# Kernel optimization log

Hardware: AMD Instinct MI355X
Metric: run time of the kernel (lower is better)

The kernel has to match this reference:

```python
import jax, jax.numpy as jnp
import numpy as np

DECAY = 0.6
GAIN = 0.4


def _layernorm(x, g, b, eps=1e-5):
    m = x.mean(-1, keepdims=True)
    v = x.var(-1, keepdims=True)
    return (x - m) * jax.lax.rsqrt(v + eps) * g + b


def _ema_scan(x, axis, reverse=False):
    # linear recurrence state = 0.6*state + 0.4*x as an associative scan
    a = jnp.full_like(x, DECAY)
    b = GAIN * x
    def comb(c1, c2):
        a1, b1 = c1
        a2, b2 = c2
        return a1 * a2, a2 * b1 + b2
    _, y = jax.lax.associative_scan(comb, (a, b), axis=axis, reverse=reverse)
    return y


def setup_inputs() -> dict:
    key = jax.random.key(0)
    B, H, W, D = 16, 64, 64, 384
    inner = 2 * D
    hidden = 4 * D
    ks = jax.random.split(key, 12)
    s = 0.02
    return {
        "x": jax.random.normal(ks[0], (B, H, W, D), jnp.float32),
        "n1_g": jnp.ones((D,), jnp.float32),
        "n1_b": jnp.zeros((D,), jnp.float32),
        "w_in": s * jax.random.normal(ks[1], (D, inner), jnp.float32),
        "b_in": jnp.zeros((inner,), jnp.float32),
        "k_conv": s * jax.random.normal(ks[2], (3, 3, 1, inner), jnp.float32),  # depthwise HWIO
        "on_g": jnp.ones((inner,), jnp.float32),
        "on_b": jnp.zeros((inner,), jnp.float32),
        "w_out": s * jax.random.normal(ks[3], (inner, D), jnp.float32),
        "b_out": jnp.zeros((D,), jnp.float32),
        "n2_g": jnp.ones((D,), jnp.float32),
        "n2_b": jnp.zeros((D,), jnp.float32),
        "w1": s * jax.random.normal(ks[4], (D, hidden), jnp.float32),
        "b1": jnp.zeros((hidden,), jnp.float32),
        "w2": s * jax.random.normal(ks[5], (hidden, D), jnp.float32),
        "b2": jnp.zeros((D,), jnp.float32),
    }


def reference(x, n1_g, n1_b, w_in, b_in, k_conv, on_g, on_b, w_out, b_out,
              n2_g, n2_b, w1, b1, w2, b2):
    inner = w_in.shape[1]
    # --- LegacyScan2DOperator branch ---
    h = _layernorm(x, n1_g, n1_b)
    p = h @ w_in + b_in  # [B,H,W,inner]
    local = jax.lax.conv_general_dilated(
        p, k_conv, window_strides=(1, 1), padding="SAME",
        dimension_numbers=("NHWC", "HWIO", "NHWC"),
        feature_group_count=inner)
    lr = _ema_scan(local, axis=2)                 # left->right over W
    rl = _ema_scan(local, axis=2, reverse=True)   # right->left
    tb = _ema_scan(local, axis=1)                 # top->bottom over H
    bt = _ema_scan(local, axis=1, reverse=True)   # bottom->top
    mixed = 0.25 * (lr + rl + tb + bt) + local
    mixed = _layernorm(mixed, on_g, on_b)
    x = x + (mixed @ w_out + b_out)
    # --- MLP branch ---
    h2 = _layernorm(x, n2_g, n2_b)
    m = jax.nn.gelu(h2 @ w1 + b1, approximate=False) @ w2 + b2
    return x + m
```

## Files before the change

kernel.cpp:

```cpp
#include <hip/hip_runtime.h>
#include <math.h>


typedef __attribute__((ext_vector_type(8))) short bf16x8;
typedef __attribute__((ext_vector_type(4))) float f32x4;

#define T_TOKENS 65536
#define DMODEL 384
#define DINNER 768
#define DHIDDEN 1536

__device__ __forceinline__ float bf2f(unsigned short u) {
  unsigned int x = ((unsigned int)u) << 16;
  return __builtin_bit_cast(float, x);
}
__device__ __forceinline__ unsigned short f2bf(float f) {
  unsigned int x = __builtin_bit_cast(unsigned int, f);
  x += 0x7fffu + ((x >> 16) & 1u);
  return (unsigned short)(x >> 16);
}
__device__ __forceinline__ void unpack2(unsigned int u, float& lo, float& hi) {
  lo = __builtin_bit_cast(float, u << 16);
  hi = __builtin_bit_cast(float, u & 0xffff0000u);
}
__device__ __forceinline__ unsigned int pack2(float lo, float hi) {
  return (unsigned int)f2bf(lo) | ((unsigned int)f2bf(hi) << 16);
}

__device__ __forceinline__ void gload16(const void* g, void* l) {
  __builtin_amdgcn_global_load_lds(
      (const __attribute__((address_space(1))) void*)g,
      (__attribute__((address_space(3))) void*)l, 16, 0, 0);
}

__global__ __launch_bounds__(256) void ln_fused_f32_384(
    const float* __restrict__ in, const float* __restrict__ g,
    const float* __restrict__ b, unsigned short* __restrict__ out) {
  const int tok = blockIdx.x * 4 + (threadIdx.x >> 6);
  const int lane = threadIdx.x & 63;
  const float2* row = (const float2*)(in + (size_t)tok * 384);
  float2 v[3];
  float s = 0.f, ss = 0.f;
#pragma unroll
  for (int k = 0; k < 3; k++) {
    v[k] = row[lane + 64 * k];
    s += v[k].x + v[k].y;
    ss += v[k].x * v[k].x + v[k].y * v[k].y;
  }
#pragma unroll
  for (int off = 32; off > 0; off >>= 1) {
    s += __shfl_xor(s, off);
    ss += __shfl_xor(ss, off);
  }
  const float m = s * (1.0f / 384.0f);
  const float r = rsqrtf(ss * (1.0f / 384.0f) - m * m + 1e-5f);
  unsigned int* op = (unsigned int*)(out + (size_t)tok * 384);
#pragma unroll
  for (int k = 0; k < 3; k++) {
    const int c = lane + 64 * k;
    const float2 gg = ((const float2*)g)[c];
    const float2 bb = ((const float2*)b)[c];
    op[c] = pack2((v[k].x - m) * r * gg.x + bb.x, (v[k].y - m) * r * gg.y + bb.y);
  }
}

__global__ __launch_bounds__(256) void ln_bundle_768(
    const uint4* __restrict__ mixed, const float* __restrict__ g,
    const float* __restrict__ b, uint4* __restrict__ out) {
  const int tid = threadIdx.x;
  const int tk = tid >> 2, j = tid & 3;
  const int token = blockIdx.x * 64 + tk;
  const int bb_ = token >> 12, posb = token & 4095;
  const size_t slab = (size_t)bb_ * 4096 + posb;
  float s = 0.f, ss = 0.f;
#pragma unroll 1
  for (int cg = j; cg < 96; cg += 4) {
    const uint4 v = mixed[((size_t)cg * 16) * 4096 + slab];
    float e0, e1, e2, e3, e4, e5, e6, e7;
    unpack2(v.x, e0, e1); unpack2(v.y, e2, e3);
    unpack2(v.z, e4, e5); unpack2(v.w, e6, e7);
    s += (e0 + e1) + (e2 + e3) + (e4 + e5) + (e6 + e7);
    ss += e0 * e0 + e1 * e1 + e2 * e2 + e3 * e3 + e4 * e4 + e5 * e5 +
          e6 * e6 + e7 * e7;
  }
  s += __shfl_xor(s, 1); ss += __shfl_xor(ss, 1);
  s += __shfl_xor(s, 2); ss += __shfl_xor(ss, 2);
  const float m = s * (1.0f / 768.0f);
  const float r = rsqrtf(ss * (1.0f / 768.0f) - m * m + 1e-5f);
  const size_t tokbase = (size_t)token * 96;
#pragma unroll 1
  for (int cg = j; cg < 96; cg += 4) {
    const uint4 v = mixed[((size_t)cg * 16) * 4096 + slab];
    const float4 g0 = *(const float4*)(g + cg * 8);
    const float4 g1 = *(const float4*)(g + cg * 8 + 4);
    const float4 b0 = *(const float4*)(b + cg * 8);
    const float4 b1 = *(const float4*)(b + cg * 8 + 4);
    float e0, e1, e2, e3, e4, e5, e6, e7;
    unpack2(v.x, e0, e1); unpack2(v.y, e2, e3);
    unpack2(v.z, e4, e5); unpack2(v.w, e6, e7);
    uint4 o;
    o.x = pack2((e0 - m) * r * g0.x + b0.x, (e1 - m) * r * g0.y + b0.y);
    o.y = pack2((e2 - m) * r * g0.z + b0.z, (e3 - m) * r * g0.w + b0.w);
    o.z = pack2((e4 - m) * r * g1.x + b1.x, (e5 - m) * r * g1.y + b1.y);
    o.w = pack2((e6 - m) * r * g1.z + b1.z, (e7 - m) * r * g1.w + b1.w);
    out[tokbase + cg] = o;
  }
}

__global__ __launch_bounds__(256) void wprep_kernel(const float* __restrict__ in,
                                                    unsigned short* __restrict__ out,
                                                    int K, int N) {
  __shared__ float t[32][33];
  const int k0 = blockIdx.x * 32, n0 = blockIdx.y * 32;
  const int a = threadIdx.x & 31, b8 = threadIdx.x >> 5;
#pragma unroll
  for (int i = 0; i < 4; i++)
    t[b8 + 8 * i][a] = in[(size_t)(k0 + b8 + 8 * i) * N + n0 + a];
  __syncthreads();
#pragma unroll
  for (int i = 0; i < 4; i++)
    out[(size_t)(n0 + b8 + 8 * i) * K + k0 + a] = f2bf(t[a][b8 + 8 * i]);
}

template <int EPI>
__global__ __launch_bounds__(256) void gemm_bt_kernel(
    const unsigned short* __restrict__ A, int lda,
    const unsigned short* __restrict__ Bt, int ldb, int KT,
    const float* __restrict__ bias, const float* __restrict__ res,
    void* __restrict__ C, int ldc, int nby) {
  __shared__ unsigned short smem[32768];
  char* const smc = (char*)smem;

  const int tid = threadIdx.x;
  const int w = tid >> 6, lane = tid & 63;
  const int cpx = gridDim.x >> 3;
  const int g = blockIdx.x;
  const int sw = (g & 7) * cpx + (g >> 3);
  const int bx = sw / nby, by = sw - bx * nby;
  const int tok0 = bx << 7, n0 = by << 7;

  const int wm = w >> 1, wn = w & 1;
  const int lrow = lane & 15, kgrp = lane >> 4;
  const int cx = lrow & 7;

  const int lr8 = lane >> 3;
  const int kce = ((lane & 7) ^ lr8) << 3;
  const unsigned short* Abase = A + (size_t)(tok0 + w * 32 + lr8) * lda + kce;
  const unsigned short* Bbase = Bt + (size_t)(n0 + w * 32 + lr8) * ldb + kce;

  f32x4 acc[4][4];
#pragma unroll
  for (int i = 0; i < 4; i++)
#pragma unroll
    for (int j = 0; j < 4; j++) {
      f32x4 z = {0.f, 0.f, 0.f, 0.f};
      acc[i][j] = z;
    }

  const int nt = KT >> 6;
#pragma unroll
  for (int i = 0; i < 4; i++) {
    gload16(Abase + (size_t)i * 8 * lda, smc + (w * 4 + i) * 1024);
    gload16(Bbase + (size_t)i * 8 * ldb, smc + 32768 + (w * 4 + i) * 1024);
  }
  __syncthreads();

  int buf = 0;
  for (int t = 0; t < nt; t++) {
    if (t + 1 < nt) {
      const int kt = (t + 1) << 6;
      const int bo = (buf ^ 1) * 16384;
#pragma unroll
      for (int i = 0; i < 4; i++) {
        gload16(Abase + (size_t)i * 8 * lda + kt, smc + bo + (w * 4 + i) * 1024);
        gload16(Bbase + (size_t)i * 8 * ldb + kt,
                smc + 32768 + bo + (w * 4 + i) * 1024);
      }
    }
    bf16x8 af[2][4], bf_[2][4];
    const int bo = buf * 16384;
#pragma unroll
    for (int ks = 0; ks < 2; ks++) {
#pragma unroll
      for (int f = 0; f < 4; f++) {
        const int co = ((ks * 4 + kgrp) ^ cx) << 4;
        af[ks][f] =
            *(const bf16x8*)(smc + bo + (wm * 64 + f * 16 + lrow) * 128 + co);
        bf_[ks][f] = *(const bf16x8*)(smc + 32768 + bo +
                                      (wn * 64 + f * 16 + lrow) * 128 + co);
      }
    }
#pragma unroll
    for (int ks = 0; ks < 2; ks++)
#pragma unroll
      for (int mf = 0; mf < 4; mf++)
#pragma unroll
        for (int nf = 0; nf < 4; nf++)
          acc[mf][nf] = __builtin_amdgcn_mfma_f32_16x16x32_bf16(
              af[ks][mf], bf_[ks][nf], acc[mf][nf], 0, 0, 0);
    __syncthreads();
    buf ^= 1;
  }

  if constexpr (EPI == 3) {
#pragma unroll
    for (int mf = 0; mf < 4; mf++)
#pragma unroll
      for (int nf = 0; nf < 4; nf++) {
        const int cl = wn * 64 + nf * 16 + lrow;
        const float bv = bias[n0 + cl];
#pragma unroll
        for (int r = 0; r < 4; r++) {
          const int tl = wm * 64 + mf * 16 + kgrp * 4 + r;
          smem[(cl >> 3) * 1032 + tl * 8 + (cl & 7)] =
              f2bf(acc[mf][nf][r] + bv);
        }
      }
    __syncthreads();
    const int bb_ = tok0 >> 12, pos0 = tok0 & 4095, cg0 = n0 >> 3;
    uint4* Cb = (uint4*)C;
#pragma unroll
    for (int e = 0; e < 8; e++) {
      const int lin = e * 256 + tid;
      const int cgl = lin >> 7, pp = lin & 127;
      const uint4 v = *(const uint4*)&smem[cgl * 1032 + pp * 8];
      Cb[((size_t)(cg0 + cgl) * 16 + bb_) * 4096 + pos0 + pp] = v;
    }
  } else {
#pragma unroll
    for (int mf = 0; mf < 4; mf++) {
#pragma unroll
      for (int nf = 0; nf < 4; nf++) {
        const int gcol = n0 + wn * 64 + nf * 16 + lrow;
        const float bv = bias ? bias[gcol] : 0.0f;
#pragma unroll
        for (int r = 0; r < 4; r++) {
          const int grow = tok0 + wm * 64 + mf * 16 + kgrp * 4 + r;
          float v = acc[mf][nf][r] + bv;
          const size_t idx = (size_t)grow * ldc + gcol;
          if constexpr (EPI == 1) {
            ((float*)C)[idx] = v + res[idx];
          } else {
            const float z = 1.5957691216057308f * (v + 0.044715f * v * v * v);
            const float gl = v / (1.0f + __expf(-z));
            ((unsigned short*)C)[idx] = f2bf(gl);
          }
        }
      }
    }
  }
}

__global__ __launch_bounds__(512) void conv_scan_kernel(
    const uint4* __restrict__ p, const float* __restrict__ kconv,
    uint4* __restrict__ mixed) {
  __shared__ unsigned int loc[4][64][65];
  __shared__ float klds[72];
  const int tid = threadIdx.x;
  const int cg = blockIdx.x;
  const int b = blockIdx.y;
  const uint4* pb = p + ((size_t)cg * 16 + b) * 4096;

  if (tid < 72) klds[tid] = kconv[(tid >> 3) * DINNER + cg * 8 + (tid & 7)];
  __syncthreads();

#pragma unroll 1
  for (int i = 0; i < 8; i++) {
    const int pos = tid + 512 * i;
    const int h = pos >> 6, w = pos & 63;
    float acc[8];
#pragma unroll
    for (int j = 0; j < 8; j++) acc[j] = 0.f;
#pragma unroll
    for (int dh = 0; dh < 3; dh++) {
      const int hh = h + dh - 1;
      const bool vh = (unsigned)hh < 64u;
      const int hcl = min(max(hh, 0), 63);
#pragma unroll
      for (int dw = 0; dw < 3; dw++) {
        const int ww = w + dw - 1;
        const bool vv = vh && ((unsigned)ww < 64u);
        const int wcl = min(max(ww, 0), 63);
        uint4 pv = pb[hcl * 64 + wcl];
        if (!vv) { pv.x = 0; pv.y = 0; pv.z = 0; pv.w = 0; }
        const int t = dh * 3 + dw;
        float lo, hi;
        unpack2(pv.x, lo, hi);
        acc[0] += lo * klds[t * 8 + 0]; acc[1] += hi * klds[t * 8 + 1];
        unpack2(pv.y, lo, hi);
        acc[2] += lo * klds[t * 8 + 2]; acc[3] += hi * klds[t * 8 + 3];
        unpack2(pv.z, lo, hi);
        acc[4] += lo * klds[t * 8 + 4]; acc[5] += hi * klds[t * 8 + 5];
        unpack2(pv.w, lo, hi);
        acc[6] += lo * klds[t * 8 + 6]; acc[7] += hi * klds[t * 8 + 7];
      }
    }
    loc[0][h][w] = pack2(acc[0], acc[1]);
    loc[1][h][w] = pack2(acc[2], acc[3]);
    loc[2][h][w] = pack2(acc[4], acc[5]);
    loc[3][h][w] = pack2(acc[6], acc[7]);
  }
  __syncthreads();

  const int grp = tid >> 8;
  const int r_ = tid & 255;
  const int ax = r_ & 63;
  const int cp = r_ >> 6;

  if (grp == 0) {
    unsigned int hc[64];
    float ya = 0.f, yb = 0.f;
#pragma unroll
    for (int h = 0; h < 64; h++) {
      float a, bv;
      unpack2(loc[cp][h][ax], a, bv);
      ya = 0.6f * ya + 0.4f * a;
      yb = 0.6f * yb + 0.4f * bv;
      hc[h] = pack2(ya, yb);
    }
    ya = 0.f; yb = 0.f;
#pragma unroll
    for (int h = 63; h >= 0; h--) {
      float a, bv, fa, fb;
      unpack2(loc[cp][h][ax], a, bv);
      ya = 0.6f * ya + 0.4f * a;
      yb = 0.6f * yb + 0.4f * bv;
      unpack2(hc[h], fa, fb);
      hc[h] = pack2(0.25f * (fa + ya), 0.25f * (fb + yb));
    }
    __syncthreads();
    __syncthreads();
#pragma unroll
    for (int h = 0; h < 64; h++) {
      float a, bv, ca, cb;
      unpack2(loc[cp][h][ax], a, bv);
      unpack2(hc[h], ca, cb);
      loc[cp][h][ax] = pack2(a + ca, bv + cb);
    }
  } else {
    unsigned int wt[64];
    float ya = 0.f, yb = 0.f;
#pragma unroll
    for (int w = 0; w < 64; w++) {
      float a, bv;
      unpack2(loc[cp][ax][w], a, bv);
      ya = 0.6f * ya + 0.4f * a;
      yb = 0.6f * yb + 0.4f * bv;
      wt[w] = pack2(ya, yb);
    }
    ya = 0.f; yb = 0.f;
#pragma unroll
    for (int w = 63; w >= 0; w--) {
      float a, bv, fa, fb;
      unpack2(loc[cp][ax][w], a, bv);
      ya = 0.6f * ya + 0.4f * a;
      yb = 0.6f * yb + 0.4f * bv;
      unpack2(wt[w], fa, fb);
      wt[w] = pack2(a + 0.25f * (fa + ya), bv + 0.25f * (fb + yb));
    }
    __syncthreads();
#pragma unroll
    for (int w = 0; w < 64; w++) loc[cp][ax][w] = wt[w];
    __syncthreads();
  }
  __syncthreads();

  uint4* mb = mixed + ((size_t)cg * 16 + b) * 4096;
#pragma unroll 1
  for (int i = 0; i < 8; i++) {
    const int pos = tid + 512 * i;
    const int h = pos >> 6, w = pos & 63;
    uint4 st;
    st.x = loc[0][h][w];
    st.y = loc[1][h][w];
    st.z = loc[2][h][w];
    st.w = loc[3][h][w];
    mb[pos] = st;
  }
}

extern "C" void kernel_launch(void* const* d_in, const int* in_sizes, int n_in,
                              void* d_out, int out_size, void* d_ws,
                              size_t ws_size, hipStream_t stream) {
  const float* x = (const float*)d_in[0];
  const float* n1_g = (const float*)d_in[1];
  const float* n1_b = (const float*)d_in[2];
  const float* w_in = (const float*)d_in[3];
  const float* b_in = (const float*)d_in[4];
  const float* k_conv = (const float*)d_in[5];
  const float* on_g = (const float*)d_in[6];
  const float* on_b = (const float*)d_in[7];
  const float* w_out = (const float*)d_in[8];
  const float* b_out = (const float*)d_in[9];
  const float* n2_g = (const float*)d_in[10];
  const float* n2_b = (const float*)d_in[11];
  const float* w1 = (const float*)d_in[12];
  const float* b1 = (const float*)d_in[13];
  const float* w2 = (const float*)d_in[14];
  const float* b2 = (const float*)d_in[15];

  const size_t MB = 1024 * 1024;
  char* ws = (char*)d_ws;
  unsigned short* R1 = (unsigned short*)(ws + 3 * MB / 2);
  unsigned short* R2 = (unsigned short*)(ws + 3 * MB / 2 + 96 * MB);

  unsigned short* A1 = R2;
  unsigned short* wTin = R2 + (48 * MB) / 2;
  unsigned short* p = R1;
  unsigned short* A2 = R2;
  unsigned short* wTout = R1;
  unsigned short* A3 = R1;
  unsigned short* wT1 = R1 + (48 * MB) / 2;
  unsigned short* wT2 = wT1 + (size_t)1536 * 384;
  unsigned short* gb = R2;

  float* out = (float*)d_out;
  dim3 b256(256);

  ln_fused_f32_384<<<T_TOKENS / 4, b256, 0, stream>>>(x, n1_g, n1_b, A1);
  wprep_kernel<<<dim3(12, 24), b256, 0, stream>>>(w_in, wTin, DMODEL, DINNER);
  gemm_bt_kernel<3><<<3072, b256, 0, stream>>>(A1, DMODEL, wTin, DMODEL, DMODEL,
                                               b_in, nullptr, p, DINNER, 6);
  conv_scan_kernel<<<dim3(96, 16), dim3(512), 0, stream>>>(
      (const uint4*)p, k_conv, (uint4*)p);
  ln_bundle_768<<<1024, b256, 0, stream>>>((const uint4*)p, on_g, on_b,
                                           (uint4*)A2);
  wprep_kernel<<<dim3(24, 12), b256, 0, stream>>>(w_out, wTout, DINNER, DMODEL);
  gemm_bt_kernel<1><<<1536, b256, 0, stream>>>(A2, DINNER, wTout, DINNER, DINNER,
                                               b_out, x, out, DMODEL, 3);
  ln_fused_f32_384<<<T_TOKENS / 4, b256, 0, stream>>>(out, n2_g, n2_b, A3);
  wprep_kernel<<<dim3(12, 48), b256, 0, stream>>>(w1, wT1, DMODEL, DHIDDEN);
  wprep_kernel<<<dim3(48, 12), b256, 0, stream>>>(w2, wT2, DHIDDEN, DMODEL);
  for (int hh = 0; hh < 2; hh++) {
    const size_t toff = (size_t)hh * 32768;
    gemm_bt_kernel<2><<<3072, b256, 0, stream>>>(
        A3 + toff * DMODEL, DMODEL, wT1, DMODEL, DMODEL, b1, nullptr, gb,
        DHIDDEN, 12);
    gemm_bt_kernel<1><<<768, b256, 0, stream>>>(
        gb, DHIDDEN, wT2, DHIDDEN, DHIDDEN, b2, out + toff * DMODEL,
        out + toff * DMODEL, DMODEL, 3);
  }
}
```

Baseline: 749.1 us.

## Parallelize EMA scans across 4 lane segments with shuffle-based carry propagation

Each 64-long EMA scan line is split into four 16-element segments, each handled by its own lane. Segment carries are combined across lanes with shuffles using precomputed powers of the decay (0.6^16, 0.6^32). The block grows to 1024 threads so the H and W scans run one after the other, each using all threads, instead of two thread groups each owning one direction with 64-entry register arrays. This cuts per-thread serial latency and register pressure. In exchange the loc data is re-read from LDS several times, and each segment takes an extra pass to build its carries.

Result: slower. 875.9 us (+16.9%).

```diff
diff --git a/kernel.cpp b/kernel.cpp
--- a/kernel.cpp
+++ b/kernel.cpp
@@ -251,7 +251,59 @@
   }
 }
 
-__global__ __launch_bounds__(512) void conv_scan_kernel(
+__device__ __forceinline__ void ema_seg(const unsigned int* __restrict__ base,
+                                        const int stride, const int seg,
+                                        unsigned int res[16]) {
+  const float A16 = 2.8211099e-4f;
+  const float A32 = 7.9586611e-8f;
+  float a, bv, t;
+  float za = 0.f, zb = 0.f;
+#pragma unroll
+  for (int j = 0; j < 16; j++) {
+    unpack2(base[j * stride], a, bv);
+    za = 0.6f * za + 0.4f * a;
+    zb = 0.6f * zb + 0.4f * bv;
+  }
+  t = __shfl_up(za, 1); if (seg >= 1) za += A16 * t;
+  t = __shfl_up(zb, 1); if (seg >= 1) zb += A16 * t;
+  t = __shfl_up(za, 2); if (seg >= 2) za += A32 * t;
+  t = __shfl_up(zb, 2); if (seg >= 2) zb += A32 * t;
+  float yfa = __shfl_up(za, 1), yfb = __shfl_up(zb, 1);
+  if (seg == 0) { yfa = 0.f; yfb = 0.f; }
+  float ua = 0.f, ub = 0.f;
+#pragma unroll
+  for (int j = 15; j >= 0; j--) {
+    unpack2(base[j * stride], a, bv);
+    ua = 0.6f * ua + 0.4f * a;
+    ub = 0.6f * ub + 0.4f * bv;
+  }
+  t = __shfl_down(ua, 1); if (seg <= 2) ua += A16 * t;
+  t = __shfl_down(ub, 1); if (seg <= 2) ub += A16 * t;
+  t = __shfl_down(ua, 2); if (seg <= 1) ua += A32 * t;
+  t = __shfl_down(ub, 2); if (seg <= 1) ub += A32 * t;
+  float zba = __shfl_down(ua, 1), zbb = __shfl_down(ub, 1);
+  if (seg == 3) { zba = 0.f; zbb = 0.f; }
+  float fa = yfa, fb = yfb;
+#pragma unroll
+  for (int j = 0; j < 16; j++) {
+    unpack2(base[j * stride], a, bv);
+    fa = 0.6f * fa + 0.4f * a;
+    fb = 0.6f * fb + 0.4f * bv;
+    res[j] = pack2(fa, fb);
+  }
+  float ga = zba, gb = zbb;
+#pragma unroll
+  for (int j = 15; j >= 0; j--) {
+    unpack2(base[j * stride], a, bv);
+    ga = 0.6f * ga + 0.4f * a;
+    gb = 0.6f * gb + 0.4f * bv;
+    float ffa, ffb;
+    unpack2(res[j], ffa, ffb);
+    res[j] = pack2(0.25f * (ffa + ga), 0.25f * (ffb + gb));
+  }
+}
+
+__global__ __launch_bounds__(1024, 4) void conv_scan_kernel(
     const uint4* __restrict__ p, const float* __restrict__ kconv,
     uint4* __restrict__ mixed) {
   __shared__ unsigned int loc[4][64][65];
@@ -265,8 +317,8 @@
   __syncthreads();
 
 #pragma unroll 1
-  for (int i = 0; i < 8; i++) {
-    const int pos = tid + 512 * i;
+  for (int i = 0; i < 4; i++) {
+    const int pos = tid + 1024 * i;
     const int h = pos >> 6, w = pos & 63;
     float acc[8];
 #pragma unroll
@@ -302,73 +354,41 @@
   }
   __syncthreads();
 
-  const int grp = tid >> 8;
-  const int r_ = tid & 255;
-  const int ax = r_ & 63;
-  const int cp = r_ >> 6;
-
-  if (grp == 0) {
-    unsigned int hc[64];
-    float ya = 0.f, yb = 0.f;
-#pragma unroll
-    for (int h = 0; h < 64; h++) {
-      float a, bv;
-      unpack2(loc[cp][h][ax], a, bv);
-      ya = 0.6f * ya + 0.4f * a;
-      yb = 0.6f * yb + 0.4f * bv;
-      hc[h] = pack2(ya, yb);
-    }
-    ya = 0.f; yb = 0.f;
-#pragma unroll
-    for (int h = 63; h >= 0; h--) {
-      float a, bv, fa, fb;
-      unpack2(loc[cp][h][ax], a, bv);
-      ya = 0.6f * ya + 0.4f * a;
-      yb = 0.6f * yb + 0.4f * bv;
-      unpack2(hc[h], fa, fb);
-      hc[h] = pack2(0.25f * (fa + ya), 0.25f * (fb + yb));
-    }
-    __syncthreads();
-    __syncthreads();
-#pragma unroll
-    for (int h = 0; h < 64; h++) {
-      float a, bv, ca, cb;
-      unpack2(loc[cp][h][ax], a, bv);
-      unpack2(hc[h], ca, cb);
-      loc[cp][h][ax] = pack2(a + ca, bv + cb);
-    }
-  } else {
-    unsigned int wt[64];
-    float ya = 0.f, yb = 0.f;
-#pragma unroll
-    for (int w = 0; w < 64; w++) {
-      float a, bv;
-      unpack2(loc[cp][ax][w], a, bv);
-      ya = 0.6f * ya + 0.4f * a;
-      yb = 0.6f * yb + 0.4f * bv;
-      wt[w] = pack2(ya, yb);
-    }
-    ya = 0.f; yb = 0.f;
-#pragma unroll
-    for (int w = 63; w >= 0; w--) {
-      float a, bv, fa, fb;
-      unpack2(loc[cp][ax][w], a, bv);
-      ya = 0.6f * ya + 0.4f * a;
-      yb = 0.6f * yb + 0.4f * bv;
-      unpack2(wt[w], fa, fb);
-      wt[w] = pack2(a + 0.25f * (fa + ya), bv + 0.25f * (fb + yb));
-    }
-    __syncthreads();
-#pragma unroll
-    for (int w = 0; w < 64; w++) loc[cp][ax][w] = wt[w];
-    __syncthreads();
+  const int seg = tid & 3;
+  const int ax = (tid >> 2) & 63;
+  const int cp = tid >> 8;
+  const int j0 = seg * 16;
+
+  unsigned int hcon[16];
+  ema_seg(&loc[cp][j0][ax], 65, seg, hcon);
+  __syncthreads();
+
+  {
+    unsigned int wcon[16];
+    ema_seg(&loc[cp][ax][j0], 1, seg, wcon);
+#pragma unroll
+    for (int j = 0; j < 16; j++) {
+      float a, bv, ra, rb;
+      unpack2(loc[cp][ax][j0 + j], a, bv);
+      unpack2(wcon[j], ra, rb);
+      loc[cp][ax][j0 + j] = pack2(a + ra, bv + rb);
+    }
+  }
+  __syncthreads();
+
+#pragma unroll
+  for (int j = 0; j < 16; j++) {
+    float a, bv, ra, rb;
+    unpack2(loc[cp][j0 + j][ax], a, bv);
+    unpack2(hcon[j], ra, rb);
+    loc[cp][j0 + j][ax] = pack2(a + ra, bv + rb);
   }
   __syncthreads();
 
   uint4* mb = mixed + ((size_t)cg * 16 + b) * 4096;
 #pragma unroll 1
-  for (int i = 0; i < 8; i++) {
-    const int pos = tid + 512 * i;
+  for (int i = 0; i < 4; i++) {
+    const int pos = tid + 1024 * i;
     const int h = pos >> 6, w = pos & 63;
     uint4 st;
     st.x = loc[0][h][w];
@@ -421,7 +441,7 @@
   wprep_kernel<<<dim3(12, 24), b256, 0, stream>>>(w_in, wTin, DMODEL, DINNER);
   gemm_bt_kernel<3><<<3072, b256, 0, stream>>>(A1, DMODEL, wTin, DMODEL, DMODEL,
                                                b_in, nullptr, p, DINNER, 6);
-  conv_scan_kernel<<<dim3(96, 16), dim3(512), 0, stream>>>(
+  conv_scan_kernel<<<dim3(96, 16), dim3(1024), 0, stream>>>(
       (const uint4*)p, k_conv, (uint4*)p);
   ln_bundle_768<<<1024, b256, 0, stream>>>((const uint4*)p, on_g, on_b,
                                            (uint4*)A2);
```
